# Kernel optimization log

Hardware: AMD Instinct MI355X
Metric: run time of the kernel (lower is better)

Reference implementation:

```python
import jax, jax.numpy as jnp
import numpy as np

# Hard-coded electrode groupings from the torch module
REGIONS = [[0, 1, 16, 17], [2, 18, 19], [3, 4], [20], [7, 8], [21, 25, 26], [5, 22],
           [6, 23, 24], [9, 27], [11], [29], [10, 15, 28], [12, 30], [13, 14, 31]]
R = 14          # number of regions
T = 4           # max region length (ragged lens 1..4, padded)
LENS = np.array([len(r) for r in REGIONS])
REG_IDX = np.array([r + [r[-1]] * (T - len(r)) for r in REGIONS])   # [R,T] padded gather indices
LAST_IDX = np.array([r[-1] for r in REGIONS])                        # last electrode per region
MASKS = (np.arange(T)[:, None] < LENS[None, :])                      # [T,R] valid-step mask

B, E, H = 8192, 128, 128   # batch, eeg_size, hidden per direction (output_size=2H=256)
G = 4 * H                  # gate width (i,f,g,o)


def setup_inputs() -> dict:
    key = jax.random.key(0)
    ks = jax.random.split(key, 5)
    s = 1.0 / np.sqrt(H)   # matches torch LSTM uniform(-1/sqrt(H),1/sqrt(H)) scale
    return {
        "x": jax.random.normal(ks[0], (B, 32, E), jnp.float32),
        "w_ih": jax.random.normal(ks[1], (R, 2, G, E), jnp.float32) * s,
        "w_hh": jax.random.normal(ks[2], (R, 2, G, H), jnp.float32) * s,
        "b_ih": jax.random.normal(ks[3], (R, 2, G), jnp.float32) * s,
        "b_hh": jax.random.normal(ks[4], (R, 2, G), jnp.float32) * s,
        "gamma": jnp.ones((R,), jnp.float32),
        "beta": jnp.zeros((R,), jnp.float32),
    }


def _cell(x_t, h, c, W_ih, W_hh, b):
    # x_t:[B,R,E] h,c:[B,R,H] W_ih:[R,G,E] W_hh:[R,G,H] b:[R,G]; torch gate order i,f,g,o
    gates = jnp.einsum('bre,rge->brg', x_t, W_ih) + jnp.einsum('brh,rgh->brg', h, W_hh) + b
    i, f, g, o = jnp.split(gates, 4, axis=-1)
    c_new = jax.nn.sigmoid(f) * c + jax.nn.sigmoid(i) * jnp.tanh(g)
    h_new = jax.nn.sigmoid(o) * jnp.tanh(c_new)
    return h_new, c_new


def reference(x, w_ih, w_hh, b_ih, b_hh, gamma, beta):
    xs = x[:, jnp.asarray(REG_IDX), :]              # [B,R,T,E] per-region gather (padded)
    xs_t = jnp.transpose(xs, (2, 0, 1, 3))          # [T,B,R,E]
    masks = jnp.asarray(MASKS)                      # [T,R]
    bf = b_ih[:, 0] + b_hh[:, 0]
    bb = b_ih[:, 1] + b_hh[:, 1]
    h0 = jnp.zeros((x.shape[0], R, H), x.dtype)
    c0 = h0

    # Forward direction: scan over padded time, freeze state past each region's length
    def step(carry, inp):
        h, c = carry
        x_t, m = inp
        h_n, c_n = _cell(x_t, h, c, w_ih[:, 0], w_hh[:, 0], bf)
        m_ = m[None, :, None]
        return (jnp.where(m_, h_n, h), jnp.where(m_, c_n, c)), None

    (h_fwd, _), _ = jax.lax.scan(step, (h0, c0), (xs_t, masks))

    # Backward direction output at last timestep == exactly one backward step on the last element
    x_last = x[:, jnp.asarray(LAST_IDX), :]         # [B,R,E]
    h_bwd, _ = _cell(x_last, h0, c0, w_ih[:, 1], w_hh[:, 1], bb)

    out = jnp.concatenate([h_fwd, h_bwd], axis=-1)  # [B,R,2H] == [batch, regions, output_size]

    # BatchNorm1d(num_features=R), training mode: biased var over (batch, feature)
    mean = out.mean(axis=(0, 2), keepdims=True)
    var = out.var(axis=(0, 2), keepdims=True)
    xhat = (out - mean) * jax.lax.rsqrt(var + 1e-5)
    return gamma[None, :, None] * xhat + beta[None, :, None]
```

## Files before the change

kernel.cpp:

```cpp
#include <hip/hip_runtime.h>

typedef __attribute__((ext_vector_type(8))) _Float16 half8;
typedef __attribute__((ext_vector_type(16))) float f32x16;

static __device__ const int d_LENS[14] = {4,3,2,1,2,3,2,3,2,1,1,3,2,3};
static __device__ const int d_RIDX[14][4] = {
  {0,1,16,17},{2,18,19,19},{3,4,4,4},{20,20,20,20},{7,8,8,8},{21,25,26,26},
  {5,22,22,22},{6,23,24,24},{9,27,27,27},{11,11,11,11},{29,29,29,29},
  {10,15,28,28},{12,30,30,30},{13,14,31,31}};

static __device__ const int d_nTot[8] = {64,96,96,128,128,128,128,128};
static __device__ const int d_regA[8] = {0,1,5,7,11,13,2,6};
static __device__ const int d_regB[8] = {0,12,12,3,9,10,4,8};
static __device__ const int d_boff[8] = {0,0,32,0,0,0,0,0};

__device__ __forceinline__ float sigf(float v){
  return __builtin_amdgcn_rcpf(1.0f + __expf(-v));
}
__device__ __forceinline__ float tanhf2(float v){
  return 1.0f - 2.0f*__builtin_amdgcn_rcpf(1.0f + __expf(2.0f*v));
}

__device__ __forceinline__ void gload16(const void* g, void* l){
  __builtin_amdgcn_global_load_lds((const __attribute__((address_space(1))) void*)g,
                                   (__attribute__((address_space(3))) void*)l, 16, 0, 0);
}

__device__ __forceinline__ void stage_chunk(const _Float16* __restrict__ base, int ci,
                                            char* wb, int tid){
  const char* src = (const char*)base + (size_t)ci*65536;
  #pragma unroll
  for (int i=0;i<8;i++){
    int L = i*8192 + tid*16;
    gload16(src + L, wb + L);
  }
}

__global__ void prep_w(const float* __restrict__ w_ih, const float* __restrict__ w_hh,
                       const float* __restrict__ b_ih, const float* __restrict__ b_hh,
                       _Float16* __restrict__ wih, _Float16* __restrict__ whh,
                       float* __restrict__ bias)
{
  int tid = blockIdx.x*256 + threadIdx.x;
  if (tid < 458752){
    int a = (tid >= 229376);
    const float* src = a ? w_hh : w_ih;
    _Float16* dst    = a ? whh  : wih;
    int t = (a ? (tid - 229376) : tid) * 8;
    int l  = (t>>3)&63, ks=(t>>9)&7, g=(t>>12)&3, uu=(t>>14)&1, c=(t>>15)&1, rd=t>>16;
    int v = l&31, q = l>>5;
    int n  = g*128 + c*64 + uu*32 + v;
    int k0 = q*8 + ks*16;
    const float* s = src + (size_t)rd*65536 + n*128 + k0;
    float4 a0 = *(const float4*)s;
    float4 a1 = *(const float4*)(s+4);
    half8 h;
    h[0]=(_Float16)a0.x; h[1]=(_Float16)a0.y; h[2]=(_Float16)a0.z; h[3]=(_Float16)a0.w;
    h[4]=(_Float16)a1.x; h[5]=(_Float16)a1.y; h[6]=(_Float16)a1.z; h[7]=(_Float16)a1.w;
    *(half8*)(dst + t) = h;
  } else {
    int t = tid - 458752;
    if (t < 14336){
      int rd = t >> 9, np = t & 511;
      int c = (np >> 8) & 1, uu = (np >> 7) & 1, g = (np >> 5) & 3, vv = np & 31;
      int n = g*128 + c*64 + uu*32 + vv;
      bias[t] = b_ih[rd*512 + n] + b_hh[rd*512 + n];
    }
  }
}

__global__ void prep_x(const float* __restrict__ x, _Float16* __restrict__ x16)
{
  size_t i8 = (size_t)blockIdx.x*256 + threadIdx.x;
  const float* p = x + i8*8;
  float4 a0 = *(const float4*)p;
  float4 a1 = *(const float4*)(p+4);
  half8 h;
  h[0]=(_Float16)a0.x; h[1]=(_Float16)a0.y; h[2]=(_Float16)a0.z; h[3]=(_Float16)a0.w;
  h[4]=(_Float16)a1.x; h[5]=(_Float16)a1.y; h[6]=(_Float16)a1.z; h[7]=(_Float16)a1.w;
  *(half8*)(x16 + i8*8) = h;
}

template<int XMODE, int F16OUT>
__global__ __launch_bounds__(512, 1) void lstm_k(
    const float* __restrict__ xf32, const _Float16* __restrict__ x16,
    const _Float16* __restrict__ wih, const _Float16* __restrict__ whh,
    const float* __restrict__ bias,
    _Float16* __restrict__ hout, float* __restrict__ fout,
    float* __restrict__ part)
{
  __shared__ char wb[65536];
  __shared__ char hb0[65536];
  __shared__ float red[16];

  const int tid  = threadIdx.x;
  const int lane = tid & 63;
  const int wv = tid >> 6;
  const int wr = wv >> 1;
  const int u  = wv & 1;
  const int v  = lane & 31;
  const int q  = lane >> 5;

  const int xcd = blockIdx.x & 7;
  const int kk  = blockIdx.x >> 3;
  if (kk >= d_nTot[xcd]) return;
  int r, bt;
  if (kk < 64){ r = d_regA[xcd]; bt = kk; }
  else        { r = d_regB[xcd]; bt = d_boff[xcd] + (kk - 64); }
  const int b0 = bt << 7;
  const int len = d_LENS[r];

  float bf[2][4];
  #pragma unroll
  for (int c=0;c<2;c++)
    #pragma unroll
    for (int g=0;g<4;g++)
      bf[c][g] = bias[(size_t)r*1024 + c*256 + u*128 + g*32 + v];

  float cst[2][16];
  #pragma unroll
  for (int c=0;c<2;c++)
    #pragma unroll
    for (int e=0;e<16;e++) cst[c][e] = 0.0f;

  half8 xa0,xa1,xa2,xa3,xa4,xa5,xa6,xa7;
  float lsum = 0.0f, lsq = 0.0f;
  const int hrow = wr*32 + v;
  char* const wp = wb + ((u*32)<<10) + (lane<<4);

#define SB() __builtin_amdgcn_sched_barrier(0)
#define GXS(KS, AR) { \
    half8 b0 = *(const half8*)(wp + ((0*8+KS)<<10)); \
    half8 b1 = *(const half8*)(wp + ((1*8+KS)<<10)); \
    half8 b2 = *(const half8*)(wp + ((2*8+KS)<<10)); \
    half8 b3 = *(const half8*)(wp + ((3*8+KS)<<10)); \
    acc0 = __builtin_amdgcn_mfma_f32_32x32x16_f16(AR, b0, acc0, 0,0,0); \
    acc1 = __builtin_amdgcn_mfma_f32_32x32x16_f16(AR, b1, acc1, 0,0,0); \
    acc2 = __builtin_amdgcn_mfma_f32_32x32x16_f16(AR, b2, acc2, 0,0,0); \
    acc3 = __builtin_amdgcn_mfma_f32_32x32x16_f16(AR, b3, acc3, 0,0,0); }
#define HXS(KS) { \
    half8 ah = *(const half8*)(hbr + ((hrow*256 + KS*32 + q*16) ^ ((hrow&15)<<4))); \
    half8 b0 = *(const half8*)(wp + ((0*8+KS)<<10)); \
    half8 b1 = *(const half8*)(wp + ((1*8+KS)<<10)); \
    half8 b2 = *(const half8*)(wp + ((2*8+KS)<<10)); \
    half8 b3 = *(const half8*)(wp + ((3*8+KS)<<10)); \
    acc0 = __builtin_amdgcn_mfma_f32_32x32x16_f16(ah, b0, acc0, 0,0,0); \
    acc1 = __builtin_amdgcn_mfma_f32_32x32x16_f16(ah, b1, acc1, 0,0,0); \
    acc2 = __builtin_amdgcn_mfma_f32_32x32x16_f16(ah, b2, acc2, 0,0,0); \
    acc3 = __builtin_amdgcn_mfma_f32_32x32x16_f16(ah, b3, acc3, 0,0,0); }

  for (int t=0; t<len; ++t){
    const int chan = d_RIDX[r][t];
    if (XMODE){
      const _Float16* xb = x16 + (((size_t)(b0 + wr*32 + v))*32 + chan)*128 + q*8;
      xa0 = *(const half8*)(xb);       xa1 = *(const half8*)(xb + 16);
      xa2 = *(const half8*)(xb + 32);  xa3 = *(const half8*)(xb + 48);
      xa4 = *(const half8*)(xb + 64);  xa5 = *(const half8*)(xb + 80);
      xa6 = *(const half8*)(xb + 96);  xa7 = *(const half8*)(xb + 112);
    } else {
      const float* xb = xf32 + (((size_t)(b0 + wr*32 + v))*32 + chan)*128 + q*8;
      #define LXF(DST, OFF) { \
        float4 a0 = *(const float4*)(xb + OFF); \
        float4 a1 = *(const float4*)(xb + OFF + 4); \
        half8 a; \
        a[0]=(_Float16)a0.x; a[1]=(_Float16)a0.y; a[2]=(_Float16)a0.z; a[3]=(_Float16)a0.w; \
        a[4]=(_Float16)a1.x; a[5]=(_Float16)a1.y; a[6]=(_Float16)a1.z; a[7]=(_Float16)a1.w; \
        DST = a; }
      LXF(xa0,0) LXF(xa1,16) LXF(xa2,32) LXF(xa3,48)
      LXF(xa4,64) LXF(xa5,80) LXF(xa6,96) LXF(xa7,112)
      #undef LXF
    }
    const bool last = (t == len-1);
    char* hbr = hb0 + (((t+1)&1) << 15);
    char* hbw = hb0 + ((t&1) << 15);

    #pragma unroll
    for (int c=0;c<2;c++){
      f32x16 acc0, acc1, acc2, acc3;
      #pragma unroll
      for (int e=0;e<16;e++){
        acc0[e] = bf[c][0]; acc1[e] = bf[c][1];
        acc2[e] = bf[c][2]; acc3[e] = bf[c][3];
      }

      __syncthreads();
      stage_chunk(wih, r*4 + c, wb, tid);
      __syncthreads();
      GXS(0,xa0) GXS(1,xa1) SB();
      GXS(2,xa2) GXS(3,xa3) SB();
      GXS(4,xa4) GXS(5,xa5) SB();
      GXS(6,xa6) GXS(7,xa7) SB();
      if (t > 0){
        __syncthreads();
        stage_chunk(whh, r*4 + c, wb, tid);
        __syncthreads();
        HXS(0) HXS(1) SB();
        HXS(2) HXS(3) SB();
        HXS(4) HXS(5) SB();
        HXS(6) HXS(7) SB();
      }
      const int ccol = c*64 + u*32 + v;
      #pragma unroll
      for (int e=0;e<16;e++){
        float iv = acc0[e], fv = acc1[e];
        float gv = acc2[e], ov = acc3[e];
        float cn = sigf(iv)*tanhf2(gv) + sigf(fv)*cst[c][e];
        cst[c][e] = cn;
        float hv = sigf(ov)*tanhf2(cn);
        _Float16 hh = (_Float16)hv;
        int rl = wr*32 + (e&3) + ((e>>2)<<3) + (q<<2);
        *(_Float16*)(hbw + ((rl*256 + ccol*2) ^ ((rl&15)<<4))) = hh;
        if (last){
          float hr = (float)hh;
          lsum += hr; lsq += hr*hr;
        }
      }
    }
  }

  {
    char* hbk = hb0 + ((len&1) << 15);
    #pragma unroll
    for (int c=0;c<2;c++){
      f32x16 acc0, acc1, acc2, acc3;
      {
        float g0 = bias[(size_t)r*1024 + 512 + c*256 + u*128 + 0*32 + v];
        float g1 = bias[(size_t)r*1024 + 512 + c*256 + u*128 + 1*32 + v];
        float g2 = bias[(size_t)r*1024 + 512 + c*256 + u*128 + 2*32 + v];
        float g3 = bias[(size_t)r*1024 + 512 + c*256 + u*128 + 3*32 + v];
        #pragma unroll
        for (int e=0;e<16;e++){
          acc0[e] = g0; acc1[e] = g1; acc2[e] = g2; acc3[e] = g3;
        }
      }
      __syncthreads();
      stage_chunk(wih, r*4 + 2 + c, wb, tid);
      __syncthreads();
      GXS(0,xa0) GXS(1,xa1) SB();
      GXS(2,xa2) GXS(3,xa3) SB();
      GXS(4,xa4) GXS(5,xa5) SB();
      GXS(6,xa6) GXS(7,xa7) SB();
      const int ccol = c*64 + u*32 + v;
      #pragma unroll
      for (int e=0;e<16;e++){
        float iv = acc0[e];
        float gv = acc2[e], ov = acc3[e];
        float cn = sigf(iv)*tanhf2(gv);
        float hv = sigf(ov)*tanhf2(cn);
        _Float16 hh = (_Float16)hv;
        int rl = wr*32 + (e&3) + ((e>>2)<<3) + (q<<2);
        *(_Float16*)(hbk + ((rl*256 + ccol*2) ^ ((rl&15)<<4))) = hh;
        float hr = (float)hh;
        lsum += hr; lsq += hr*hr;
      }
    }
  }
#undef GXS
#undef HXS
#undef SB

  __syncthreads();
  {
    const char* hf  = hb0 + (((len-1)&1) << 15);
    const char* hbk = hb0 + ((len&1) << 15);
    #pragma unroll
    for (int i=0;i<4;i++){
      int row = (tid>>4) + i*32;
      int bo  = (tid&15)*16;
      int lp  = row*256 + (bo ^ ((row&15)<<4));
      uint4 df = *(const uint4*)(hf + lp);
      uint4 db = *(const uint4*)(hbk + lp);
      size_t ob = ((size_t)(b0+row)*14 + r)*256;
      if (F16OUT){
        *(uint4*)((char*)hout + ob*2 + bo)       = df;
        *(uint4*)((char*)hout + ob*2 + 256 + bo) = db;
      } else {
        const _Float16* pf = (const _Float16*)&df;
        const _Float16* pb = (const _Float16*)&db;
        float* of  = fout + ob + (bo>>1);
        float* obw = fout + ob + 128 + (bo>>1);
        float4 o0, o1;
        o0.x=(float)pf[0]; o0.y=(float)pf[1]; o0.z=(float)pf[2]; o0.w=(float)pf[3];
        o1.x=(float)pf[4]; o1.y=(float)pf[5]; o1.z=(float)pf[6]; o1.w=(float)pf[7];
        *(float4*)of = o0; *(float4*)(of+4) = o1;
        o0.x=(float)pb[0]; o0.y=(float)pb[1]; o0.z=(float)pb[2]; o0.w=(float)pb[3];
        o1.x=(float)pb[4]; o1.y=(float)pb[5]; o1.z=(float)pb[6]; o1.w=(float)pb[7];
        *(float4*)obw = o0; *(float4*)(obw+4) = o1;
      }
    }
  }

  #pragma unroll
  for (int off=32; off>0; off>>=1){
    lsum += __shfl_down(lsum, off);
    lsq  += __shfl_down(lsq, off);
  }
  __syncthreads();
  if (lane == 0){ red[wv] = lsum; red[8+wv] = lsq; }
  __syncthreads();
  if (tid == 0){
    float s = 0.0f, s2 = 0.0f;
    #pragma unroll
    for (int ww=0;ww<8;ww++){ s += red[ww]; s2 += red[8+ww]; }
    part[((size_t)r*64 + bt)*2]     = s;
    part[((size_t)r*64 + bt)*2 + 1] = s2;
  }
}

__global__ void stats_k(const float* __restrict__ part, const float* __restrict__ gamma,
                        const float* __restrict__ beta, float* __restrict__ stat)
{
  int r = blockIdx.x, l = threadIdx.x;
  float s  = part[((size_t)r*64 + l)*2];
  float s2 = part[((size_t)r*64 + l)*2 + 1];
  #pragma unroll
  for (int off=32; off>0; off>>=1){ s += __shfl_down(s, off); s2 += __shfl_down(s2, off); }
  if (l == 0){
    const float cnt = 2097152.0f;
    float m = s / cnt;
    float var = s2 / cnt - m*m;
    float rstd = rsqrtf(var + 1e-5f);
    float sc = gamma[r]*rstd;
    stat[r*2]   = sc;
    stat[r*2+1] = beta[r] - m*sc;
  }
}

__global__ void apply_f16(const _Float16* __restrict__ hst, const float* __restrict__ stat,
                          float* __restrict__ out)
{
  size_t i8 = (size_t)blockIdx.x*256 + threadIdx.x;
  uint4 vv = *(const uint4*)(hst + i8*8);
  int r = (int)((i8 >> 5) % 14);
  float sc = stat[r*2], sh = stat[r*2+1];
  const _Float16* hp = (const _Float16*)&vv;
  float4 o0, o1;
  o0.x = (float)hp[0]*sc + sh; o0.y = (float)hp[1]*sc + sh;
  o0.z = (float)hp[2]*sc + sh; o0.w = (float)hp[3]*sc + sh;
  o1.x = (float)hp[4]*sc + sh; o1.y = (float)hp[5]*sc + sh;
  o1.z = (float)hp[6]*sc + sh; o1.w = (float)hp[7]*sc + sh;
  ((float4*)out)[i8*2]     = o0;
  ((float4*)out)[i8*2 + 1] = o1;
}

__global__ void apply_f32(float* __restrict__ out, const float* __restrict__ stat)
{
  size_t idx = (size_t)blockIdx.x*256 + threadIdx.x;
  float4* p = (float4*)out + idx;
  float4 vv = *p;
  int r = (int)((idx >> 6) % 14);
  float sc = stat[r*2], sh = stat[r*2+1];
  vv.x = vv.x*sc + sh; vv.y = vv.y*sc + sh; vv.z = vv.z*sc + sh; vv.w = vv.w*sc + sh;
  *p = vv;
}

extern "C" void kernel_launch(void* const* d_in, const int* in_sizes, int n_in,
                              void* d_out, int out_size, void* d_ws, size_t ws_size,
                              hipStream_t stream)
{
  const float* x     = (const float*)d_in[0];
  const float* w_ih  = (const float*)d_in[1];
  const float* w_hh  = (const float*)d_in[2];
  const float* b_ih  = (const float*)d_in[3];
  const float* b_hh  = (const float*)d_in[4];
  const float* gamma = (const float*)d_in[5];
  const float* beta  = (const float*)d_in[6];
  float* out = (float*)d_out;

  const size_t HS = 29360128;
  const size_t XS = 33554432;
  const size_t wbytes = (size_t)1835008*2;
  const size_t tail = (14336 + 1792 + 28)*4;
  const size_t need_full = XS*2 + HS*2 + 2*wbytes + tail;

  char* wsp = (char*)d_ws;
  int full = (ws_size >= need_full) ? 1 : 0;

  _Float16* x16p; _Float16* hstore; _Float16* wihp;
  if (full){
    x16p   = (_Float16*)wsp;
    hstore = (_Float16*)(wsp + XS*2);
    wihp   = (_Float16*)(wsp + XS*2 + HS*2);
  } else {
    x16p   = (_Float16*)wsp;
    hstore = (_Float16*)wsp;
    wihp   = (_Float16*)wsp;
  }
  _Float16* whhp = wihp + 1835008;
  float* biasp = (float*)(whhp + 1835008);
  float* partp = biasp + 14336;
  float* statp = partp + 1792;

  prep_w<<<1848, 256, 0, stream>>>(w_ih, w_hh, b_ih, b_hh, wihp, whhp, biasp);
  if (full){
    prep_x<<<16384, 256, 0, stream>>>(x, x16p);
    lstm_k<1,1><<<1024, 512, 0, stream>>>(x, x16p, wihp, whhp, biasp,
                                          hstore, out, partp);
  } else {
    lstm_k<0,0><<<1024, 512, 0, stream>>>(x, x16p, wihp, whhp, biasp,
                                          hstore, out, partp);
  }
  stats_k<<<14, 64, 0, stream>>>(partp, gamma, beta, statp);
  if (full)
    apply_f16<<<14336, 256, 0, stream>>>(hstore, statp, out);
  else
    apply_f32<<<28672, 256, 0, stream>>>(out, statp);
}
```

Baseline: 405.0 us.

## Read LSTM weight fragments directly from global memory, halve block batch tile

Result: slower. 705.1 us (+74.1%).

```diff
diff --git a/kernel.cpp b/kernel.cpp
--- a/kernel.cpp
+++ b/kernel.cpp
@@ -9,31 +9,16 @@
   {5,22,22,22},{6,23,24,24},{9,27,27,27},{11,11,11,11},{29,29,29,29},
   {10,15,28,28},{12,30,30,30},{13,14,31,31}};
 
-static __device__ const int d_nTot[8] = {64,96,96,128,128,128,128,128};
+static __device__ const int d_nTot[8] = {128,192,192,256,256,256,256,256};
 static __device__ const int d_regA[8] = {0,1,5,7,11,13,2,6};
 static __device__ const int d_regB[8] = {0,12,12,3,9,10,4,8};
-static __device__ const int d_boff[8] = {0,0,32,0,0,0,0,0};
+static __device__ const int d_boff[8] = {0,0,64,0,0,0,0,0};
 
 __device__ __forceinline__ float sigf(float v){
   return __builtin_amdgcn_rcpf(1.0f + __expf(-v));
 }
 __device__ __forceinline__ float tanhf2(float v){
   return 1.0f - 2.0f*__builtin_amdgcn_rcpf(1.0f + __expf(2.0f*v));
-}
-
-__device__ __forceinline__ void gload16(const void* g, void* l){
-  __builtin_amdgcn_global_load_lds((const __attribute__((address_space(1))) void*)g,
-                                   (__attribute__((address_space(3))) void*)l, 16, 0, 0);
-}
-
-__device__ __forceinline__ void stage_chunk(const _Float16* __restrict__ base, int ci,
-                                            char* wb, int tid){
-  const char* src = (const char*)base + (size_t)ci*65536;
-  #pragma unroll
-  for (int i=0;i<8;i++){
-    int L = i*8192 + tid*16;
-    gload16(src + L, wb + L);
-  }
 }
 
 __global__ void prep_w(const float* __restrict__ w_ih, const float* __restrict__ w_hh,
@@ -82,15 +67,14 @@
 }
 
 template<int XMODE, int F16OUT>
-__global__ __launch_bounds__(512, 1) void lstm_k(
+__global__ __launch_bounds__(256, 1) void lstm_k(
     const float* __restrict__ xf32, const _Float16* __restrict__ x16,
     const _Float16* __restrict__ wih, const _Float16* __restrict__ whh,
     const float* __restrict__ bias,
     _Float16* __restrict__ hout, float* __restrict__ fout,
     float* __restrict__ part)
 {
-  __shared__ char wb[65536];
-  __shared__ char hb0[65536];
+  __shared__ char hb0[32768];
   __shared__ float red[16];
 
   const int tid  = threadIdx.x;
@@ -105,9 +89,9 @@
   const int kk  = blockIdx.x >> 3;
   if (kk >= d_nTot[xcd]) return;
   int r, bt;
-  if (kk < 64){ r = d_regA[xcd]; bt = kk; }
-  else        { r = d_regB[xcd]; bt = d_boff[xcd] + (kk - 64); }
-  const int b0 = bt << 7;
+  if (kk < 128){ r = d_regA[xcd]; bt = kk; }
+  else         { r = d_regB[xcd]; bt = d_boff[xcd] + (kk - 128); }
+  const int b0 = bt << 6;
   const int len = d_LENS[r];
 
   float bf[2][4];
@@ -126,24 +110,23 @@
   half8 xa0,xa1,xa2,xa3,xa4,xa5,xa6,xa7;
   float lsum = 0.0f, lsq = 0.0f;
   const int hrow = wr*32 + v;
-  char* const wp = wb + ((u*32)<<10) + (lane<<4);
 
 #define SB() __builtin_amdgcn_sched_barrier(0)
-#define GXS(KS, AR) { \
-    half8 b0 = *(const half8*)(wp + ((0*8+KS)<<10)); \
-    half8 b1 = *(const half8*)(wp + ((1*8+KS)<<10)); \
-    half8 b2 = *(const half8*)(wp + ((2*8+KS)<<10)); \
-    half8 b3 = *(const half8*)(wp + ((3*8+KS)<<10)); \
+#define GXS(WP, KS, AR) { \
+    half8 b0 = *(const half8*)(WP + (0*8+KS)*512); \
+    half8 b1 = *(const half8*)(WP + (1*8+KS)*512); \
+    half8 b2 = *(const half8*)(WP + (2*8+KS)*512); \
+    half8 b3 = *(const half8*)(WP + (3*8+KS)*512); \
     acc0 = __builtin_amdgcn_mfma_f32_32x32x16_f16(AR, b0, acc0, 0,0,0); \
     acc1 = __builtin_amdgcn_mfma_f32_32x32x16_f16(AR, b1, acc1, 0,0,0); \
     acc2 = __builtin_amdgcn_mfma_f32_32x32x16_f16(AR, b2, acc2, 0,0,0); \
     acc3 = __builtin_amdgcn_mfma_f32_32x32x16_f16(AR, b3, acc3, 0,0,0); }
-#define HXS(KS) { \
+#define HXS(WP, KS) { \
     half8 ah = *(const half8*)(hbr + ((hrow*256 + KS*32 + q*16) ^ ((hrow&15)<<4))); \
-    half8 b0 = *(const half8*)(wp + ((0*8+KS)<<10)); \
-    half8 b1 = *(const half8*)(wp + ((1*8+KS)<<10)); \
-    half8 b2 = *(const half8*)(wp + ((2*8+KS)<<10)); \
-    half8 b3 = *(const half8*)(wp + ((3*8+KS)<<10)); \
+    half8 b0 = *(const half8*)(WP + (0*8+KS)*512); \
+    half8 b1 = *(const half8*)(WP + (1*8+KS)*512); \
+    half8 b2 = *(const half8*)(WP + (2*8+KS)*512); \
+    half8 b3 = *(const half8*)(WP + (3*8+KS)*512); \
     acc0 = __builtin_amdgcn_mfma_f32_32x32x16_f16(ah, b0, acc0, 0,0,0); \
     acc1 = __builtin_amdgcn_mfma_f32_32x32x16_f16(ah, b1, acc1, 0,0,0); \
     acc2 = __builtin_amdgcn_mfma_f32_32x32x16_f16(ah, b2, acc2, 0,0,0); \
@@ -171,8 +154,8 @@
       #undef LXF
     }
     const bool last = (t == len-1);
-    char* hbr = hb0 + (((t+1)&1) << 15);
-    char* hbw = hb0 + ((t&1) << 15);
+    char* hbr = hb0 + (((t+1)&1) << 14);
+    char* hbw = hb0 + ((t&1) << 14);
 
     #pragma unroll
     for (int c=0;c<2;c++){
@@ -182,22 +165,19 @@
         acc0[e] = bf[c][0]; acc1[e] = bf[c][1];
         acc2[e] = bf[c][2]; acc3[e] = bf[c][3];
       }
-
-      __syncthreads();
-      stage_chunk(wih, r*4 + c, wb, tid);
-      __syncthreads();
-      GXS(0,xa0) GXS(1,xa1) SB();
-      GXS(2,xa2) GXS(3,xa3) SB();
-      GXS(4,xa4) GXS(5,xa5) SB();
-      GXS(6,xa6) GXS(7,xa7) SB();
+      {
+        const _Float16* wp = wih + (size_t)(r*4 + c)*32768 + u*16384 + lane*8;
+        GXS(wp,0,xa0) GXS(wp,1,xa1) SB();
+        GXS(wp,2,xa2) GXS(wp,3,xa3) SB();
+        GXS(wp,4,xa4) GXS(wp,5,xa5) SB();
+        GXS(wp,6,xa6) GXS(wp,7,xa7) SB();
+      }
       if (t > 0){
-        __syncthreads();
-        stage_chunk(whh, r*4 + c, wb, tid);
-        __syncthreads();
-        HXS(0) HXS(1) SB();
-        HXS(2) HXS(3) SB();
-        HXS(4) HXS(5) SB();
-        HXS(6) HXS(7) SB();
+        const _Float16* wp = whh + (size_t)(r*4 + c)*32768 + u*16384 + lane*8;
+        HXS(wp,0) HXS(wp,1) SB();
+        HXS(wp,2) HXS(wp,3) SB();
+        HXS(wp,4) HXS(wp,5) SB();
+        HXS(wp,6) HXS(wp,7) SB();
       }
       const int ccol = c*64 + u*32 + v;
       #pragma unroll
@@ -216,10 +196,12 @@
         }
       }
     }
+    if (!last) __syncthreads();
   }
 
   {
-    char* hbk = hb0 + ((len&1) << 15);
+    char* hbk = hb0 + ((len&1) << 14);
+    __syncthreads();
     #pragma unroll
     for (int c=0;c<2;c++){
       f32x16 acc0, acc1, acc2, acc3;
@@ -233,13 +215,11 @@
           acc0[e] = g0; acc1[e] = g1; acc2[e] = g2; acc3[e] = g3;
         }
       }
-      __syncthreads();
-      stage_chunk(wih, r*4 + 2 + c, wb, tid);
-      __syncthreads();
-      GXS(0,xa0) GXS(1,xa1) SB();
-      GXS(2,xa2) GXS(3,xa3) SB();
-      GXS(4,xa4) GXS(5,xa5) SB();
-      GXS(6,xa6) GXS(7,xa7) SB();
+      const _Float16* wp = wih + (size_t)(r*4 + 2 + c)*32768 + u*16384 + lane*8;
+      GXS(wp,0,xa0) GXS(wp,1,xa1) SB();
+      GXS(wp,2,xa2) GXS(wp,3,xa3) SB();
+      GXS(wp,4,xa4) GXS(wp,5,xa5) SB();
+      GXS(wp,6,xa6) GXS(wp,7,xa7) SB();
       const int ccol = c*64 + u*32 + v;
       #pragma unroll
       for (int e=0;e<16;e++){
@@ -261,11 +241,11 @@
 
   __syncthreads();
   {
-    const char* hf  = hb0 + (((len-1)&1) << 15);
-    const char* hbk = hb0 + ((len&1) << 15);
+    const char* hf  = hb0 + (((len-1)&1) << 14);
+    const char* hbk = hb0 + ((len&1) << 14);
     #pragma unroll
     for (int i=0;i<4;i++){
-      int row = (tid>>4) + i*32;
+      int row = (tid>>4) + i*16;
       int bo  = (tid&15)*16;
       int lp  = row*256 + (bo ^ ((row&15)<<4));
       uint4 df = *(const uint4*)(hf + lp);
@@ -301,9 +281,9 @@
   if (tid == 0){
     float s = 0.0f, s2 = 0.0f;
     #pragma unroll
-    for (int ww=0;ww<8;ww++){ s += red[ww]; s2 += red[8+ww]; }
-    part[((size_t)r*64 + bt)*2]     = s;
-    part[((size_t)r*64 + bt)*2 + 1] = s2;
+    for (int ww=0;ww<4;ww++){ s += red[ww]; s2 += red[8+ww]; }
+    part[((size_t)r*128 + bt)*2]     = s;
+    part[((size_t)r*128 + bt)*2 + 1] = s2;
   }
 }
 
@@ -311,8 +291,8 @@
                         const float* __restrict__ beta, float* __restrict__ stat)
 {
   int r = blockIdx.x, l = threadIdx.x;
-  float s  = part[((size_t)r*64 + l)*2];
-  float s2 = part[((size_t)r*64 + l)*2 + 1];
+  float s  = part[((size_t)r*128 + l)*2]       + part[((size_t)r*128 + 64 + l)*2];
+  float s2 = part[((size_t)r*128 + l)*2 + 1]   + part[((size_t)r*128 + 64 + l)*2 + 1];
   #pragma unroll
   for (int off=32; off>0; off>>=1){ s += __shfl_down(s, off); s2 += __shfl_down(s2, off); }
   if (l == 0){
@@ -370,7 +350,7 @@
   const size_t HS = 29360128;
   const size_t XS = 33554432;
   const size_t wbytes = (size_t)1835008*2;
-  const size_t tail = (14336 + 1792 + 28)*4;
+  const size_t tail = (14336 + 3584 + 28)*4;
   const size_t need_full = XS*2 + HS*2 + 2*wbytes + tail;
 
   char* wsp = (char*)d_ws;
@@ -389,15 +369,15 @@
   _Float16* whhp = wihp + 1835008;
   float* biasp = (float*)(whhp + 1835008);
   float* partp = biasp + 14336;
-  float* statp = partp + 1792;
+  float* statp = partp + 3584;
 
   prep_w<<<1848, 256, 0, stream>>>(w_ih, w_hh, b_ih, b_hh, wihp, whhp, biasp);
   if (full){
     prep_x<<<16384, 256, 0, stream>>>(x, x16p);
-    lstm_k<1,1><<<1024, 512, 0, stream>>>(x, x16p, wihp, whhp, biasp,
+    lstm_k<1,1><<<2048, 256, 0, stream>>>(x, x16p, wihp, whhp, biasp,
                                           hstore, out, partp);
   } else {
-    lstm_k<0,0><<<1024, 512, 0, stream>>>(x, x16p, wihp, whhp, biasp,
+    lstm_k<0,0><<<2048, 256, 0, stream>>>(x, x16p, wihp, whhp, biasp,
                                           hstore, out, partp);
   }
   stats_k<<<14, 64, 0, stream>>>(partp, gamma, beta, statp);
```
